# Performance work log

Measured on AMD Instinct MI355X. Metric: run time of the kernel, lower is better.

Reference implementation:

```python
import jax, jax.numpy as jnp
import numpy as np

WIN = 7          # window height/width
P = 10           # prompts_len
HEADS = 12
B0 = 32          # image batch (spa_prompts batch)
NW = 64          # windows per image
NW_TOK = WIN * WIN  # 49


def _relative_position_index(w):
    coords = np.stack(np.meshgrid(np.arange(w), np.arange(w), indexing='ij'))  # [2,w,w]
    flat = coords.reshape(2, -1)                        # [2, w*w]
    rel = flat[:, :, None] - flat[:, None, :]           # [2, w*w, w*w]
    rel = rel.transpose(1, 2, 0).astype(np.int64)       # [w*w, w*w, 2]
    rel[..., 0] += w - 1
    rel[..., 1] += w - 1
    rel[..., 0] *= 2 * w - 1
    return rel.sum(-1)                                  # [w*w, w*w]

REL_IDX = jnp.asarray(_relative_position_index(WIN))    # [49,49] int


def setup_inputs() -> dict:
    key = jax.random.key(0)
    ks = jax.random.split(key, 8)
    dim = 384
    return {
        'x': jax.random.normal(ks[0], (B0 * NW, NW_TOK, dim), jnp.float32),
        'spa_prompts': jax.random.normal(ks[1], (B0, P, dim), jnp.float32),
        'mask': jax.random.normal(ks[2], (NW, NW_TOK, NW_TOK), jnp.float32),
        'bias_table': jax.random.normal(ks[3], (169, HEADS), jnp.float32) * 0.02,
        'w_qkv': jax.random.normal(ks[4], (3 * dim, dim), jnp.float32) * 0.02,
        'b_qkv': jax.random.normal(ks[5], (3 * dim,), jnp.float32) * 0.02,
        'w_proj': jax.random.normal(ks[6], (dim, dim), jnp.float32) * 0.02,
        'b_proj': jax.random.normal(ks[7], (dim,), jnp.float32) * 0.02,
    }


def reference(x, spa_prompts, mask, bias_table, w_qkv, b_qkv, w_proj, b_proj):
    B_, Nw, C = x.shape
    b0 = spa_prompts.shape[0]
    nW = B_ // b0
    hd = C // HEADS
    scale = hd ** -0.5

    # broadcast prompts to every window and prepend
    prompts = jnp.broadcast_to(spa_prompts[:, None], (b0, nW, P, C)).reshape(B_, P, C)
    xc = jnp.concatenate([prompts, x], axis=1)          # [B_, N, C], N = P + Nw
    N = xc.shape[1]

    qkv = xc @ w_qkv.T + b_qkv                          # [B_, N, 3C]
    qkv = qkv.reshape(B_, N, 3, HEADS, hd).transpose(2, 0, 3, 1, 4)
    q, k, v = qkv[0], qkv[1], qkv[2]                    # [B_, H, N, hd]

    attn_weight = jnp.einsum('bhnd,bhmd->bhnm', q, k)   # unscaled, returned

    # relative position bias gathered for the window block, padded over prompt rows/cols
    rpb = bias_table[REL_IDX.reshape(-1)].reshape(NW_TOK, NW_TOK, HEADS)
    rpb = rpb.transpose(2, 0, 1)                        # [H, 49, 49]
    bias_full = jnp.pad(rpb, ((0, 0), (P, 0), (P, 0)))  # [H, N, N]

    attn = attn_weight * scale + bias_full[None]

    mask_full = jnp.pad(mask, ((0, 0), (P, 0), (P, 0)))  # [nW, N, N]
    attn = attn.reshape(b0, nW, HEADS, N, N) + mask_full[None, :, None]
    attn = jax.nn.softmax(attn.reshape(B_, HEADS, N, N), axis=-1)

    out = jnp.einsum('bhnm,bhmd->bnhd', attn, v).reshape(B_, N, C)
    out = out @ w_proj.T + b_proj

    prompts_out = out[:, :P].reshape(b0, nW, P, C).mean(axis=1)
    x_out = out[:, P:]
    return (x_out, attn_weight, prompts_out)
```

## Files before the change

kernel.cpp:

```cpp
#include <hip/hip_runtime.h>
#include <hip/hip_bf16.h>

#define P     10
#define NTOK  59
#define HEADS 12
#define NWTOK 49

#define AW_OFF 38535168
#define PO_OFF 124096512

typedef __attribute__((ext_vector_type(8))) short short8;
typedef __attribute__((ext_vector_type(8))) unsigned short ushort8;
typedef __attribute__((ext_vector_type(4))) float floatx4;
typedef unsigned int uint_g __attribute__((address_space(1)));
typedef unsigned int uint_l __attribute__((address_space(3)));

__device__ __forceinline__ unsigned short f2b(float f) {
  unsigned u = __builtin_bit_cast(unsigned, f);
  u += 0x7fffu + ((u >> 16) & 1u);
  return (unsigned short)(u >> 16);
}

__device__ __forceinline__ void gll16(const void* g, void* l) {
  __builtin_amdgcn_global_load_lds((const uint_g*)g, (uint_l*)l, 16, 0, 0);
}

__global__ __launch_bounds__(256) void convert_w_kernel(
    const float* __restrict__ w, unsigned short* __restrict__ wb) {
  const int i = (blockIdx.x * 256 + threadIdx.x) * 8;
  const float4 a = *(const float4*)(w + i);
  const float4 b = *(const float4*)(w + i + 4);
  ushort8 o;
  o[0] = f2b(a.x); o[1] = f2b(a.y); o[2] = f2b(a.z); o[3] = f2b(a.w);
  o[4] = f2b(b.x); o[5] = f2b(b.y); o[6] = f2b(b.z); o[7] = f2b(b.w);
  *(ushort8*)(wb + i) = o;
}

__global__ __launch_bounds__(256) void combo_kernel(
    const float* __restrict__ mask, const float* __restrict__ bias_table,
    float* __restrict__ combo) {
  const int bid = blockIdx.x;
  const int h = bid % HEADS, wnd = bid / HEADS;
  for (int e = threadIdx.x; e < 2401; e += 256) {
    const int ti = e / 49, tj = e - (e / 49) * 49;
    const int ai = ti / 7, aj = ti - ai * 7;
    const int bi = tj / 7, bj = tj - bi * 7;
    const int ridx = (ai - bi + 6) * 13 + (aj - bj + 6);
    combo[(size_t)bid * 2401 + e] =
        bias_table[ridx * HEADS + h] + mask[(size_t)wnd * 2401 + e];
  }
}

__global__ __launch_bounds__(256) void gather_x_kernel(
    const float* __restrict__ x, const float* __restrict__ spa,
    unsigned short* __restrict__ xc) {
  const int chunk = blockIdx.x * 256 + threadIdx.x;
  const int m = chunk / 48, kc = chunk - m * 48;
  const int b = m / 59, tok = m - b * 59;
  const float* src = (tok < P)
      ? spa + ((size_t)((b >> 6) * P + tok)) * 384 + kc * 8
      : x + ((size_t)(b * NWTOK + tok - P)) * 384 + kc * 8;
  const float4 v0 = ((const float4*)src)[0];
  const float4 v1 = ((const float4*)src)[1];
  ushort8 o;
  o[0] = f2b(v0.x); o[1] = f2b(v0.y); o[2] = f2b(v0.z); o[3] = f2b(v0.w);
  o[4] = f2b(v1.x); o[5] = f2b(v1.y); o[6] = f2b(v1.z); o[7] = f2b(v1.w);
  *(ushort8*)(xc + (size_t)m * 384 + kc * 8) = o;
}

__global__ __launch_bounds__(256) void gemm_qkv_kernel(
    const unsigned short* __restrict__ A, const unsigned short* __restrict__ Bw,
    const float* __restrict__ b_qkv, unsigned short* __restrict__ qkvw) {
  __shared__ unsigned short Asw[8192];
  __shared__ unsigned short Bsw[8192];
  const int t = threadIdx.x;
  const int w = t >> 6, lane = t & 63;
  const int lr = lane & 15, lg = lane >> 4;
  const int w0 = w >> 1, w1 = w & 1;
  const size_t m0 = (size_t)blockIdx.y * 128;
  const int n0 = blockIdx.x * 128;
  const int srow = lane >> 3, cpos = lane & 7;

  floatx4 acc[4][4];
#pragma unroll
  for (int mr = 0; mr < 4; ++mr)
#pragma unroll
    for (int nc = 0; nc < 4; ++nc) acc[mr][nc] = (floatx4)0.f;

  for (int k0 = 0; k0 < 384; k0 += 64) {
#pragma unroll
    for (int i = 0; i < 4; ++i) {
      const int r = (w * 4 + i) * 8 + srow;
      const int c = cpos ^ (r & 7);
      gll16(A + (m0 + r) * 384 + k0 + c * 8, Asw + (w * 4 + i) * 512);
      gll16(Bw + (size_t)(n0 + r) * 384 + k0 + c * 8, Bsw + (w * 4 + i) * 512);
    }
    __syncthreads();
#pragma unroll
    for (int kh = 0; kh < 2; ++kh) {
      short8 af[4], bf[4];
#pragma unroll
      for (int mr = 0; mr < 4; ++mr) {
        const int r = w0 * 64 + mr * 16 + lr;
        af[mr] = *(const short8*)(Asw + r * 64 + (((kh * 4 + lg) ^ (r & 7)) * 8));
      }
#pragma unroll
      for (int nc = 0; nc < 4; ++nc) {
        const int r = w1 * 64 + nc * 16 + lr;
        bf[nc] = *(const short8*)(Bsw + r * 64 + (((kh * 4 + lg) ^ (r & 7)) * 8));
      }
#pragma unroll
      for (int mr = 0; mr < 4; ++mr)
#pragma unroll
        for (int nc = 0; nc < 4; ++nc)
          acc[mr][nc] = __builtin_amdgcn_mfma_f32_16x16x32_bf16(
              af[mr], bf[nc], acc[mr][nc], 0, 0, 0);
    }
    __syncthreads();
  }

  const int sec = blockIdx.x / 3;
  float bias[4]; int hh[4], dd[4];
#pragma unroll
  for (int nc = 0; nc < 4; ++nc) {
    const int n = n0 + w1 * 64 + nc * 16 + lr;
    bias[nc] = b_qkv[n];
    hh[nc] = (n >> 5) % 12;
    dd[nc] = n & 31;
  }
#pragma unroll
  for (int mr = 0; mr < 4; ++mr)
#pragma unroll
    for (int reg = 0; reg < 4; ++reg) {
      const int m = (int)m0 + w0 * 64 + mr * 16 + lg * 4 + reg;
      const int bb = m / 59, tok = m - bb * 59;
      const size_t base = (size_t)(bb * 3 + sec) * 12 * 1888 + (size_t)tok * 32;
#pragma unroll
      for (int nc = 0; nc < 4; ++nc)
        qkvw[base + (size_t)hh[nc] * 1888 + dd[nc]] =
            f2b(acc[mr][nc][reg] + bias[nc]);
    }
}

__global__ __launch_bounds__(256) void attn_kernel(
    const unsigned short* __restrict__ qkvw, const float* __restrict__ combo,
    float* __restrict__ aw_out, unsigned short* __restrict__ attn_bf) {
  __shared__ char lds[31872];
  float* S = (float*)lds;
  unsigned short* qs = (unsigned short*)(lds + 16896);
  unsigned short* ks = (unsigned short*)(lds + 22016);
  unsigned short* vt = (unsigned short*)(lds + 27136);
  unsigned short* Pm = (unsigned short*)(lds + 16896);

  const int blk = blockIdx.x;
  const int b = blk / HEADS, h = blk - b * HEADS;
  const int t = threadIdx.x;
  const int w = t >> 6, lane = t & 63, lr = lane & 15, lg = lane >> 4;

  const size_t qoff = ((size_t)(b * 3 + 0) * 12 + h) * 1888;
  const size_t koff = ((size_t)(b * 3 + 1) * 12 + h) * 1888;
  const size_t voff = ((size_t)(b * 3 + 2) * 12 + h) * 1888;

  if (t < 236) {
    const int row = t >> 2, dc = (t & 3) * 8;
    const ushort8 q8 = *(const ushort8*)(qkvw + qoff + t * 8);
    const ushort8 k8 = *(const ushort8*)(qkvw + koff + t * 8);
    const ushort8 v8 = *(const ushort8*)(qkvw + voff + t * 8);
    *(ushort8*)(qs + row * 40 + dc) = q8;
    *(ushort8*)(ks + row * 40 + dc) = k8;
#pragma unroll
    for (int j = 0; j < 8; ++j) vt[(dc + j) * 74 + row] = v8[j];
  } else {
    const int e = t - 236;
#pragma unroll
    for (int jj = 0; jj < 8; ++jj) {
      const int f = e * 8 + jj;
      vt[(f / 5) * 74 + 59 + (f % 5)] = 0;
    }
  }
  __syncthreads();

  const short8 qa = *(const short8*)(qs + (w * 16 + lr) * 40 + lg * 8);
  const int q = w * 16 + lr;
  floatx4 sacc[4];
#pragma unroll
  for (int nt = 0; nt < 4; ++nt) {
    const short8 kb = *(const short8*)(ks + (nt * 16 + lr) * 40 + lg * 8);
    sacc[nt] = __builtin_amdgcn_mfma_f32_16x16x32_bf16(kb, qa, (floatx4)0.f, 0, 0, 0);
  }
#pragma unroll
  for (int nt = 0; nt < 4; ++nt)
#pragma unroll
    for (int reg = 0; reg < 4; ++reg)
      S[q * 66 + nt * 16 + lg * 4 + reg] = sacc[nt][reg];
  __syncthreads();

  float* aw = aw_out + (size_t)blk * (NTOK * NTOK);
  for (int idx = t; idx < NTOK * NTOK; idx += 256) {
    const int i = idx / 59, j = idx - i * 59;
    aw[idx] = S[i * 66 + j];
  }

  const float scale = 0.17677669529663687f;
  const float* comb = combo + (size_t)((b & 63) * HEADS + h) * 2401;
  float ev[4][4];
  float mx = -3.0e38f;
#pragma unroll
  for (int nt = 0; nt < 4; ++nt)
#pragma unroll
    for (int reg = 0; reg < 4; ++reg) {
      const int kk = nt * 16 + lg * 4 + reg;
      float v = -3.0e38f;
      if (q < NTOK && kk < NTOK) {
        const float cb = (q >= P && kk >= P) ? comb[(q - P) * 49 + (kk - P)] : 0.f;
        v = fmaf(sacc[nt][reg], scale, cb);
      }
      ev[nt][reg] = v;
      mx = fmaxf(mx, v);
    }
  mx = fmaxf(mx, __shfl_xor(mx, 16));
  mx = fmaxf(mx, __shfl_xor(mx, 32));
  float sm = 0.f;
#pragma unroll
  for (int nt = 0; nt < 4; ++nt)
#pragma unroll
    for (int reg = 0; reg < 4; ++reg) {
      const float e = __expf(ev[nt][reg] - mx);
      ev[nt][reg] = e;
      sm += e;
    }
  sm += __shfl_xor(sm, 16);
  sm += __shfl_xor(sm, 32);
  const float inv = 1.0f / sm;
#pragma unroll
  for (int nt = 0; nt < 4; ++nt) {
    uint2 uu;
    uu.x = (unsigned)f2b(ev[nt][0] * inv) | ((unsigned)f2b(ev[nt][1] * inv) << 16);
    uu.y = (unsigned)f2b(ev[nt][2] * inv) | ((unsigned)f2b(ev[nt][3] * inv) << 16);
    *(uint2*)(Pm + q * 72 + nt * 16 + lg * 4) = uu;
  }

  floatx4 oacc[2];
  oacc[0] = (floatx4)0.f; oacc[1] = (floatx4)0.f;
#pragma unroll
  for (int kk = 0; kk < 2; ++kk) {
    const short8 pa = *(const short8*)(Pm + (w * 16 + lr) * 72 + kk * 32 + lg * 8);
#pragma unroll
    for (int nt = 0; nt < 2; ++nt) {
      const short8 vb = *(const short8*)(vt + (nt * 16 + lr) * 74 + kk * 32 + lg * 8);
      oacc[nt] = __builtin_amdgcn_mfma_f32_16x16x32_bf16(pa, vb, oacc[nt], 0, 0, 0);
    }
  }
#pragma unroll
  for (int nt = 0; nt < 2; ++nt)
#pragma unroll
    for (int reg = 0; reg < 4; ++reg) {
      const int row = w * 16 + lg * 4 + reg;
      if (row < NTOK) {
        const int d = nt * 16 + lr;
        attn_bf[((size_t)(b * NTOK + row)) * 384 + h * 32 + d] = f2b(oacc[nt][reg]);
      }
    }
}

__global__ __launch_bounds__(256) void gemm_proj_kernel(
    const unsigned short* __restrict__ A, const unsigned short* __restrict__ Bw,
    const float* __restrict__ b_proj, float* __restrict__ x_out,
    float* __restrict__ pbuf) {
  __shared__ unsigned short Asw[8192];
  __shared__ unsigned short Bsw[8192];
  const int t = threadIdx.x;
  const int w = t >> 6, lane = t & 63;
  const int lr = lane & 15, lg = lane >> 4;
  const int w0 = w >> 1, w1 = w & 1;
  const size_t m0 = (size_t)blockIdx.y * 128;
  const int n0 = blockIdx.x * 128;
  const int srow = lane >> 3, cpos = lane & 7;

  floatx4 acc[4][4];
#pragma unroll
  for (int mr = 0; mr < 4; ++mr)
#pragma unroll
    for (int nc = 0; nc < 4; ++nc) acc[mr][nc] = (floatx4)0.f;

  for (int k0 = 0; k0 < 384; k0 += 64) {
#pragma unroll
    for (int i = 0; i < 4; ++i) {
      const int r = (w * 4 + i) * 8 + srow;
      const int c = cpos ^ (r & 7);
      gll16(A + (m0 + r) * 384 + k0 + c * 8, Asw + (w * 4 + i) * 512);
      gll16(Bw + (size_t)(n0 + r) * 384 + k0 + c * 8, Bsw + (w * 4 + i) * 512);
    }
    __syncthreads();
#pragma unroll
    for (int kh = 0; kh < 2; ++kh) {
      short8 af[4], bf[4];
#pragma unroll
      for (int mr = 0; mr < 4; ++mr) {
        const int r = w0 * 64 + mr * 16 + lr;
        af[mr] = *(const short8*)(Asw + r * 64 + (((kh * 4 + lg) ^ (r & 7)) * 8));
      }
#pragma unroll
      for (int nc = 0; nc < 4; ++nc) {
        const int r = w1 * 64 + nc * 16 + lr;
        bf[nc] = *(const short8*)(Bsw + r * 64 + (((kh * 4 + lg) ^ (r & 7)) * 8));
      }
#pragma unroll
      for (int mr = 0; mr < 4; ++mr)
#pragma unroll
        for (int nc = 0; nc < 4; ++nc)
          acc[mr][nc] = __builtin_amdgcn_mfma_f32_16x16x32_bf16(
              af[mr], bf[nc], acc[mr][nc], 0, 0, 0);
    }
    __syncthreads();
  }

  float bias[4]; int nn[4];
#pragma unroll
  for (int nc = 0; nc < 4; ++nc) {
    nn[nc] = n0 + w1 * 64 + nc * 16 + lr;
    bias[nc] = b_proj[nn[nc]];
  }
#pragma unroll
  for (int mr = 0; mr < 4; ++mr)
#pragma unroll
    for (int reg = 0; reg < 4; ++reg) {
      const int m = (int)m0 + w0 * 64 + mr * 16 + lg * 4 + reg;
      const int bb = m / 59, tok = m - bb * 59;
      float* dst = (tok >= P)
          ? x_out + (size_t)(bb * NWTOK + tok - P) * 384
          : pbuf + (size_t)(bb * P + tok) * 384;
#pragma unroll
      for (int nc = 0; nc < 4; ++nc)
        dst[nn[nc]] = acc[mr][nc][reg] + bias[nc];
    }
}

__global__ __launch_bounds__(256) void reduce_prompts_kernel(
    const float* __restrict__ pbuf, float* __restrict__ po) {
  const int o = blockIdx.x * 256 + threadIdx.x;
  const int b0 = o / 3840;
  const int rem = o - b0 * 3840;
  const float* base = pbuf + (size_t)b0 * 64 * 3840 + rem;
  float s = 0.f;
#pragma unroll 8
  for (int w = 0; w < 64; ++w) s += base[(size_t)w * 3840];
  po[o] = s * (1.f / 64.f);
}

extern "C" void kernel_launch(void* const* d_in, const int* in_sizes, int n_in,
                              void* d_out, int out_size, void* d_ws, size_t ws_size,
                              hipStream_t stream) {
  const float* x          = (const float*)d_in[0];
  const float* spa        = (const float*)d_in[1];
  const float* mask       = (const float*)d_in[2];
  const float* bias_table = (const float*)d_in[3];
  const float* w_qkv      = (const float*)d_in[4];
  const float* b_qkv      = (const float*)d_in[5];
  const float* w_proj     = (const float*)d_in[6];
  const float* b_proj     = (const float*)d_in[7];
  float* out = (float*)d_out;

  unsigned short* xc_bf    = (unsigned short*)d_ws;
  unsigned short* attn_bf  = xc_bf;
  unsigned short* qkvw     = (unsigned short*)((char*)d_ws + 92798976ULL);
  unsigned short* wqkv_bf  = (unsigned short*)((char*)d_ws + 371195904ULL);
  unsigned short* wproj_bf = (unsigned short*)((char*)d_ws + 372080640ULL);
  float*          pbuf     = (float*)((char*)d_ws + 372375552ULL);
  float*          combo    = (float*)((char*)d_ws + 403832832ULL);

  convert_w_kernel<<<216, 256, 0, stream>>>(w_qkv, wqkv_bf);
  convert_w_kernel<<<72, 256, 0, stream>>>(w_proj, wproj_bf);
  combo_kernel<<<768, 256, 0, stream>>>(mask, bias_table, combo);
  gather_x_kernel<<<22656, 256, 0, stream>>>(x, spa, xc_bf);
  gemm_qkv_kernel<<<dim3(9, 944), 256, 0, stream>>>(xc_bf, wqkv_bf, b_qkv, qkvw);
  attn_kernel<<<2048 * HEADS, 256, 0, stream>>>(qkvw, combo, out + AW_OFF, attn_bf);
  gemm_proj_kernel<<<dim3(3, 944), 256, 0, stream>>>(attn_bf, wproj_bf, b_proj,
                                                     out, pbuf);
  reduce_prompts_kernel<<<480, 256, 0, stream>>>(pbuf, out + PO_OFF);
}
```

Baseline: 604.4 us.

## Compute prompt QKV once per image instead of per window, write outputs directly

The QKV GEMM no longer runs on prompt tokens replicated across all 64 windows. It computes x tokens and the 320 unique prompt rows separately into two layouts, and the attention kernel reads prompt q/k/v from the shared per-image buffer. The attention kernel also writes the fp32 attn_weight rows straight from MFMA registers, dropping the LDS staging and its extra barrier, and stages the bf16 output through LDS so global stores are 16-byte. The cost is more branching and address logic in both kernels, plus a partially wasted tile for the prompt rows.

```diff
diff --git a/kernel.cpp b/kernel.cpp
--- a/kernel.cpp
+++ b/kernel.cpp
@@ -12,6 +12,7 @@
 typedef __attribute__((ext_vector_type(8))) short short8;
 typedef __attribute__((ext_vector_type(8))) unsigned short ushort8;
 typedef __attribute__((ext_vector_type(4))) float floatx4;
+typedef float f4u __attribute__((ext_vector_type(4), aligned(4)));
 typedef unsigned int uint_g __attribute__((address_space(1)));
 typedef unsigned int uint_l __attribute__((address_space(3)));
 
@@ -51,33 +52,18 @@
   }
 }
 
-__global__ __launch_bounds__(256) void gather_x_kernel(
-    const float* __restrict__ x, const float* __restrict__ spa,
-    unsigned short* __restrict__ xc) {
-  const int chunk = blockIdx.x * 256 + threadIdx.x;
-  const int m = chunk / 48, kc = chunk - m * 48;
-  const int b = m / 59, tok = m - b * 59;
-  const float* src = (tok < P)
-      ? spa + ((size_t)((b >> 6) * P + tok)) * 384 + kc * 8
-      : x + ((size_t)(b * NWTOK + tok - P)) * 384 + kc * 8;
-  const float4 v0 = ((const float4*)src)[0];
-  const float4 v1 = ((const float4*)src)[1];
-  ushort8 o;
-  o[0] = f2b(v0.x); o[1] = f2b(v0.y); o[2] = f2b(v0.z); o[3] = f2b(v0.w);
-  o[4] = f2b(v1.x); o[5] = f2b(v1.y); o[6] = f2b(v1.z); o[7] = f2b(v1.w);
-  *(ushort8*)(xc + (size_t)m * 384 + kc * 8) = o;
-}
-
 __global__ __launch_bounds__(256) void gemm_qkv_kernel(
-    const unsigned short* __restrict__ A, const unsigned short* __restrict__ Bw,
-    const float* __restrict__ b_qkv, unsigned short* __restrict__ qkvw) {
+    const unsigned short* __restrict__ xb, const unsigned short* __restrict__ xp,
+    const unsigned short* __restrict__ Bw, const float* __restrict__ b_qkv,
+    unsigned short* __restrict__ qkx, unsigned short* __restrict__ qkp) {
   __shared__ unsigned short Asw[8192];
   __shared__ unsigned short Bsw[8192];
   const int t = threadIdx.x;
   const int w = t >> 6, lane = t & 63;
   const int lr = lane & 15, lg = lane >> 4;
   const int w0 = w >> 1, w1 = w & 1;
-  const size_t m0 = (size_t)blockIdx.y * 128;
+  const int by = blockIdx.y;
+  const bool isP = by >= 784;
   const int n0 = blockIdx.x * 128;
   const int srow = lane >> 3, cpos = lane & 7;
 
@@ -92,7 +78,15 @@
     for (int i = 0; i < 4; ++i) {
       const int r = (w * 4 + i) * 8 + srow;
       const int c = cpos ^ (r & 7);
-      gll16(A + (m0 + r) * 384 + k0 + c * 8, Asw + (w * 4 + i) * 512);
+      const unsigned short* asrc;
+      if (!isP) {
+        asrc = xb + (size_t)(by * 128 + r) * 384 + k0 + c * 8;
+      } else {
+        int mp = (by - 784) * 128 + r;
+        if (mp > 319) mp = 319;
+        asrc = xp + (size_t)mp * 384 + k0 + c * 8;
+      }
+      gll16(asrc, Asw + (w * 4 + i) * 512);
       gll16(Bw + (size_t)(n0 + r) * 384 + k0 + c * 8, Bsw + (w * 4 + i) * 512);
     }
     __syncthreads();
@@ -132,40 +126,60 @@
   for (int mr = 0; mr < 4; ++mr)
 #pragma unroll
     for (int reg = 0; reg < 4; ++reg) {
-      const int m = (int)m0 + w0 * 64 + mr * 16 + lg * 4 + reg;
-      const int bb = m / 59, tok = m - bb * 59;
-      const size_t base = (size_t)(bb * 3 + sec) * 12 * 1888 + (size_t)tok * 32;
-#pragma unroll
-      for (int nc = 0; nc < 4; ++nc)
-        qkvw[base + (size_t)hh[nc] * 1888 + dd[nc]] =
-            f2b(acc[mr][nc][reg] + bias[nc]);
+      const int rloc = w0 * 64 + mr * 16 + lg * 4 + reg;
+      if (!isP) {
+        const int m = by * 128 + rloc;
+        const int bb = m / 49, tok = m - bb * 49;
+        const size_t base = (size_t)(bb * 3 + sec) * 12 * 1568 + (size_t)tok * 32;
+#pragma unroll
+        for (int nc = 0; nc < 4; ++nc)
+          qkx[base + (size_t)hh[nc] * 1568 + dd[nc]] =
+              f2b(acc[mr][nc][reg] + bias[nc]);
+      } else {
+        const int mp = (by - 784) * 128 + rloc;
+        if (mp < 320) {
+          const int b0 = mp / 10, ptok = mp - b0 * 10;
+          const size_t base = (size_t)(b0 * 3 + sec) * 12 * 320 + (size_t)ptok * 32;
+#pragma unroll
+          for (int nc = 0; nc < 4; ++nc)
+            qkp[base + (size_t)hh[nc] * 320 + dd[nc]] =
+                f2b(acc[mr][nc][reg] + bias[nc]);
+        }
+      }
     }
 }
 
 __global__ __launch_bounds__(256) void attn_kernel(
-    const unsigned short* __restrict__ qkvw, const float* __restrict__ combo,
-    float* __restrict__ aw_out, unsigned short* __restrict__ attn_bf) {
-  __shared__ char lds[31872];
-  float* S = (float*)lds;
-  unsigned short* qs = (unsigned short*)(lds + 16896);
-  unsigned short* ks = (unsigned short*)(lds + 22016);
-  unsigned short* vt = (unsigned short*)(lds + 27136);
-  unsigned short* Pm = (unsigned short*)(lds + 16896);
+    const unsigned short* __restrict__ qkx, const unsigned short* __restrict__ qkp,
+    const float* __restrict__ combo, float* __restrict__ aw_out,
+    unsigned short* __restrict__ attn_bf) {
+  __shared__ char lds[14976];
+  unsigned short* qs = (unsigned short*)(lds);
+  unsigned short* ks = (unsigned short*)(lds + 5120);
+  unsigned short* vt = (unsigned short*)(lds + 10240);
+  unsigned short* Pm = (unsigned short*)(lds);
 
   const int blk = blockIdx.x;
   const int b = blk / HEADS, h = blk - b * HEADS;
   const int t = threadIdx.x;
   const int w = t >> 6, lane = t & 63, lr = lane & 15, lg = lane >> 4;
 
-  const size_t qoff = ((size_t)(b * 3 + 0) * 12 + h) * 1888;
-  const size_t koff = ((size_t)(b * 3 + 1) * 12 + h) * 1888;
-  const size_t voff = ((size_t)(b * 3 + 2) * 12 + h) * 1888;
-
   if (t < 236) {
     const int row = t >> 2, dc = (t & 3) * 8;
-    const ushort8 q8 = *(const ushort8*)(qkvw + qoff + t * 8);
-    const ushort8 k8 = *(const ushort8*)(qkvw + koff + t * 8);
-    const ushort8 v8 = *(const ushort8*)(qkvw + voff + t * 8);
+    ushort8 q8, k8, v8;
+    if (row < P) {
+      const size_t base =
+          ((size_t)((b >> 6) * 3) * 12 + h) * 320 + row * 32 + dc;
+      q8 = *(const ushort8*)(qkp + base);
+      k8 = *(const ushort8*)(qkp + base + 12 * 320);
+      v8 = *(const ushort8*)(qkp + base + 24 * 320);
+    } else {
+      const size_t base =
+          ((size_t)(b * 3) * 12 + h) * 1568 + (row - P) * 32 + dc;
+      q8 = *(const ushort8*)(qkx + base);
+      k8 = *(const ushort8*)(qkx + base + 12 * 1568);
+      v8 = *(const ushort8*)(qkx + base + 24 * 1568);
+    }
     *(ushort8*)(qs + row * 40 + dc) = q8;
     *(ushort8*)(ks + row * 40 + dc) = k8;
 #pragma unroll
@@ -180,25 +194,27 @@
   }
   __syncthreads();
 
-  const short8 qa = *(const short8*)(qs + (w * 16 + lr) * 40 + lg * 8);
   const int q = w * 16 + lr;
+  const short8 qa = *(const short8*)(qs + q * 40 + lg * 8);
   floatx4 sacc[4];
 #pragma unroll
   for (int nt = 0; nt < 4; ++nt) {
     const short8 kb = *(const short8*)(ks + (nt * 16 + lr) * 40 + lg * 8);
     sacc[nt] = __builtin_amdgcn_mfma_f32_16x16x32_bf16(kb, qa, (floatx4)0.f, 0, 0, 0);
   }
-#pragma unroll
-  for (int nt = 0; nt < 4; ++nt)
-#pragma unroll
-    for (int reg = 0; reg < 4; ++reg)
-      S[q * 66 + nt * 16 + lg * 4 + reg] = sacc[nt][reg];
-  __syncthreads();
-
-  float* aw = aw_out + (size_t)blk * (NTOK * NTOK);
-  for (int idx = t; idx < NTOK * NTOK; idx += 256) {
-    const int i = idx / 59, j = idx - i * 59;
-    aw[idx] = S[i * 66 + j];
+
+  if (q < NTOK) {
+    float* rowp = aw_out + (size_t)blk * 3481 + q * 59;
+#pragma unroll
+    for (int nt = 0; nt < 3; ++nt)
+      *(f4u*)(rowp + nt * 16 + lg * 4) = __builtin_bit_cast(f4u, sacc[nt]);
+    if (lg < 2) {
+      *(f4u*)(rowp + 48 + lg * 4) = __builtin_bit_cast(f4u, sacc[3]);
+    } else if (lg == 2) {
+      rowp[56] = sacc[3][0];
+      rowp[57] = sacc[3][1];
+      rowp[58] = sacc[3][2];
+    }
   }
 
   const float scale = 0.17677669529663687f;
@@ -232,6 +248,8 @@
   sm += __shfl_xor(sm, 16);
   sm += __shfl_xor(sm, 32);
   const float inv = 1.0f / sm;
+
+  __syncthreads();
 #pragma unroll
   for (int nt = 0; nt < 4; ++nt) {
     uint2 uu;
@@ -251,16 +269,19 @@
       oacc[nt] = __builtin_amdgcn_mfma_f32_16x16x32_bf16(pa, vb, oacc[nt], 0, 0, 0);
     }
   }
+
+  unsigned short* wb = Pm + w * 1152;
 #pragma unroll
   for (int nt = 0; nt < 2; ++nt)
 #pragma unroll
-    for (int reg = 0; reg < 4; ++reg) {
-      const int row = w * 16 + lg * 4 + reg;
-      if (row < NTOK) {
-        const int d = nt * 16 + lr;
-        attn_bf[((size_t)(b * NTOK + row)) * 384 + h * 32 + d] = f2b(oacc[nt][reg]);
-      }
-    }
+    for (int reg = 0; reg < 4; ++reg)
+      wb[(lg * 4 + reg) * 40 + nt * 16 + lr] = f2b(oacc[nt][reg]);
+  const int rr = lane >> 2, c8 = (lane & 3) * 8;
+  const int row = w * 16 + rr;
+  if (row < NTOK) {
+    const ushort8 ov = *(const ushort8*)(wb + rr * 40 + c8);
+    *(ushort8*)(attn_bf + ((size_t)(b * NTOK + row)) * 384 + h * 32 + c8) = ov;
+  }
 }
 
 __global__ __launch_bounds__(256) void gemm_proj_kernel(
@@ -361,20 +382,25 @@
   const float* b_proj     = (const float*)d_in[7];
   float* out = (float*)d_out;
 
-  unsigned short* xc_bf    = (unsigned short*)d_ws;
-  unsigned short* attn_bf  = xc_bf;
-  unsigned short* qkvw     = (unsigned short*)((char*)d_ws + 92798976ULL);
-  unsigned short* wqkv_bf  = (unsigned short*)((char*)d_ws + 371195904ULL);
-  unsigned short* wproj_bf = (unsigned short*)((char*)d_ws + 372080640ULL);
-  float*          pbuf     = (float*)((char*)d_ws + 372375552ULL);
-  float*          combo    = (float*)((char*)d_ws + 403832832ULL);
-
+  unsigned short* x_bf     = (unsigned short*)d_ws;
+  unsigned short* attn_bf  = (unsigned short*)d_ws;
+  unsigned short* xp_bf    = (unsigned short*)((char*)d_ws + 77070336ULL);
+  unsigned short* wqkv_bf  = (unsigned short*)((char*)d_ws + 77316096ULL);
+  unsigned short* qkx      = (unsigned short*)((char*)d_ws + 92798976ULL);
+  unsigned short* qkp      = (unsigned short*)((char*)d_ws + 324009984ULL);
+  unsigned short* wproj_bf = (unsigned short*)((char*)d_ws + 324747264ULL);
+  float*          pbuf     = (float*)((char*)d_ws + 325042176ULL);
+  float*          combo    = (float*)((char*)d_ws + 356499456ULL);
+
+  convert_w_kernel<<<18816, 256, 0, stream>>>(x, x_bf);
+  convert_w_kernel<<<60, 256, 0, stream>>>(spa, xp_bf);
   convert_w_kernel<<<216, 256, 0, stream>>>(w_qkv, wqkv_bf);
   convert_w_kernel<<<72, 256, 0, stream>>>(w_proj, wproj_bf);
   combo_kernel<<<768, 256, 0, stream>>>(mask, bias_table, combo);
-  gather_x_kernel<<<22656, 256, 0, stream>>>(x, spa, xc_bf);
-  gemm_qkv_kernel<<<dim3(9, 944), 256, 0, stream>>>(xc_bf, wqkv_bf, b_qkv, qkvw);
-  attn_kernel<<<2048 * HEADS, 256, 0, stream>>>(qkvw, combo, out + AW_OFF, attn_bf);
+  gemm_qkv_kernel<<<dim3(9, 787), 256, 0, stream>>>(x_bf, xp_bf, wqkv_bf, b_qkv,
+                                                    qkx, qkp);
+  attn_kernel<<<2048 * HEADS, 256, 0, stream>>>(qkx, qkp, combo, out + AW_OFF,
+                                                attn_bf);
   gemm_proj_kernel<<<dim3(3, 944), 256, 0, stream>>>(attn_bf, wproj_bf, b_proj,
                                                      out, pbuf);
   reduce_prompts_kernel<<<480, 256, 0, stream>>>(pbuf, out + PO_OFF);
```

After: 594.1 us. Within noise of the previous version (-1.7%).

## Fuse input gather, QKV GEMM and attention into one per-window kernel

Applied to the files above, without the earlier changes.

Replaces the separate gather, QKV GEMM and per-head attention kernels with one kernel per window (512 threads). It converts the window's tokens to bf16 in LDS, streams the QKV weights through double-buffered LDS, and keeps Q/K/V in LDS for two rounds of six heads. This removes the large bf16 xc and qkv intermediates written to and read back from global memory, plus two launches. The trade is heavy LDS use (about 85 KB) and many accumulator registers, which may limit occupancy. Each block also rereads the full weight matrix, so weight reuse across windows now comes only from cache.

```diff
diff --git a/kernel.cpp b/kernel.cpp
--- a/kernel.cpp
+++ b/kernel.cpp
@@ -12,6 +12,7 @@
 typedef __attribute__((ext_vector_type(8))) short short8;
 typedef __attribute__((ext_vector_type(8))) unsigned short ushort8;
 typedef __attribute__((ext_vector_type(4))) float floatx4;
+typedef float f4u __attribute__((ext_vector_type(4), aligned(4)));
 typedef unsigned int uint_g __attribute__((address_space(1)));
 typedef unsigned int uint_l __attribute__((address_space(3)));
 
@@ -51,216 +52,243 @@
   }
 }
 
-__global__ __launch_bounds__(256) void gather_x_kernel(
+__global__ __launch_bounds__(512, 2) void fused_qkv_attn_kernel(
     const float* __restrict__ x, const float* __restrict__ spa,
-    unsigned short* __restrict__ xc) {
-  const int chunk = blockIdx.x * 256 + threadIdx.x;
-  const int m = chunk / 48, kc = chunk - m * 48;
-  const int b = m / 59, tok = m - b * 59;
-  const float* src = (tok < P)
-      ? spa + ((size_t)((b >> 6) * P + tok)) * 384 + kc * 8
-      : x + ((size_t)(b * NWTOK + tok - P)) * 384 + kc * 8;
-  const float4 v0 = ((const float4*)src)[0];
-  const float4 v1 = ((const float4*)src)[1];
-  ushort8 o;
-  o[0] = f2b(v0.x); o[1] = f2b(v0.y); o[2] = f2b(v0.z); o[3] = f2b(v0.w);
-  o[4] = f2b(v1.x); o[5] = f2b(v1.y); o[6] = f2b(v1.z); o[7] = f2b(v1.w);
-  *(ushort8*)(xc + (size_t)m * 384 + kc * 8) = o;
-}
-
-__global__ __launch_bounds__(256) void gemm_qkv_kernel(
-    const unsigned short* __restrict__ A, const unsigned short* __restrict__ Bw,
-    const float* __restrict__ b_qkv, unsigned short* __restrict__ qkvw) {
-  __shared__ unsigned short Asw[8192];
-  __shared__ unsigned short Bsw[8192];
-  const int t = threadIdx.x;
-  const int w = t >> 6, lane = t & 63;
-  const int lr = lane & 15, lg = lane >> 4;
-  const int w0 = w >> 1, w1 = w & 1;
-  const size_t m0 = (size_t)blockIdx.y * 128;
-  const int n0 = blockIdx.x * 128;
-  const int srow = lane >> 3, cpos = lane & 7;
-
-  floatx4 acc[4][4];
-#pragma unroll
-  for (int mr = 0; mr < 4; ++mr)
-#pragma unroll
-    for (int nc = 0; nc < 4; ++nc) acc[mr][nc] = (floatx4)0.f;
-
-  for (int k0 = 0; k0 < 384; k0 += 64) {
-#pragma unroll
-    for (int i = 0; i < 4; ++i) {
-      const int r = (w * 4 + i) * 8 + srow;
-      const int c = cpos ^ (r & 7);
-      gll16(A + (m0 + r) * 384 + k0 + c * 8, Asw + (w * 4 + i) * 512);
-      gll16(Bw + (size_t)(n0 + r) * 384 + k0 + c * 8, Bsw + (w * 4 + i) * 512);
-    }
-    __syncthreads();
-#pragma unroll
-    for (int kh = 0; kh < 2; ++kh) {
-      short8 af[4], bf[4];
-#pragma unroll
-      for (int mr = 0; mr < 4; ++mr) {
-        const int r = w0 * 64 + mr * 16 + lr;
-        af[mr] = *(const short8*)(Asw + r * 64 + (((kh * 4 + lg) ^ (r & 7)) * 8));
-      }
-#pragma unroll
-      for (int nc = 0; nc < 4; ++nc) {
-        const int r = w1 * 64 + nc * 16 + lr;
-        bf[nc] = *(const short8*)(Bsw + r * 64 + (((kh * 4 + lg) ^ (r & 7)) * 8));
-      }
-#pragma unroll
-      for (int mr = 0; mr < 4; ++mr)
-#pragma unroll
-        for (int nc = 0; nc < 4; ++nc)
-          acc[mr][nc] = __builtin_amdgcn_mfma_f32_16x16x32_bf16(
-              af[mr], bf[nc], acc[mr][nc], 0, 0, 0);
-    }
-    __syncthreads();
-  }
-
-  const int sec = blockIdx.x / 3;
-  float bias[4]; int hh[4], dd[4];
-#pragma unroll
-  for (int nc = 0; nc < 4; ++nc) {
-    const int n = n0 + w1 * 64 + nc * 16 + lr;
-    bias[nc] = b_qkv[n];
-    hh[nc] = (n >> 5) % 12;
-    dd[nc] = n & 31;
-  }
-#pragma unroll
-  for (int mr = 0; mr < 4; ++mr)
-#pragma unroll
-    for (int reg = 0; reg < 4; ++reg) {
-      const int m = (int)m0 + w0 * 64 + mr * 16 + lg * 4 + reg;
-      const int bb = m / 59, tok = m - bb * 59;
-      const size_t base = (size_t)(bb * 3 + sec) * 12 * 1888 + (size_t)tok * 32;
-#pragma unroll
-      for (int nc = 0; nc < 4; ++nc)
-        qkvw[base + (size_t)hh[nc] * 1888 + dd[nc]] =
-            f2b(acc[mr][nc][reg] + bias[nc]);
-    }
-}
-
-__global__ __launch_bounds__(256) void attn_kernel(
-    const unsigned short* __restrict__ qkvw, const float* __restrict__ combo,
-    float* __restrict__ aw_out, unsigned short* __restrict__ attn_bf) {
-  __shared__ char lds[31872];
-  float* S = (float*)lds;
-  unsigned short* qs = (unsigned short*)(lds + 16896);
-  unsigned short* ks = (unsigned short*)(lds + 22016);
-  unsigned short* vt = (unsigned short*)(lds + 27136);
-  unsigned short* Pm = (unsigned short*)(lds + 16896);
-
-  const int blk = blockIdx.x;
-  const int b = blk / HEADS, h = blk - b * HEADS;
+    const unsigned short* __restrict__ wqb, const float* __restrict__ b_qkv,
+    const float* __restrict__ combo, float* __restrict__ aw_out,
+    unsigned short* __restrict__ attn_bf) {
+  __shared__ char lds[87040];
+  unsigned short* xs   = (unsigned short*)lds;
+  unsigned short* wstA = (unsigned short*)(lds + 50176);
+  unsigned short* wstB = (unsigned short*)(lds + 66560);
+  unsigned short* q_l  = (unsigned short*)lds;
+  unsigned short* k_l  = (unsigned short*)(lds + 25600);
+  unsigned short* vt   = (unsigned short*)(lds + 51200);
+  unsigned short* obuf = (unsigned short*)(lds + 78848);
+
+  const int b = blockIdx.x;
   const int t = threadIdx.x;
   const int w = t >> 6, lane = t & 63, lr = lane & 15, lg = lane >> 4;
-
-  const size_t qoff = ((size_t)(b * 3 + 0) * 12 + h) * 1888;
-  const size_t koff = ((size_t)(b * 3 + 1) * 12 + h) * 1888;
-  const size_t voff = ((size_t)(b * 3 + 2) * 12 + h) * 1888;
-
-  if (t < 236) {
-    const int row = t >> 2, dc = (t & 3) * 8;
-    const ushort8 q8 = *(const ushort8*)(qkvw + qoff + t * 8);
-    const ushort8 k8 = *(const ushort8*)(qkvw + koff + t * 8);
-    const ushort8 v8 = *(const ushort8*)(qkvw + voff + t * 8);
-    *(ushort8*)(qs + row * 40 + dc) = q8;
-    *(ushort8*)(ks + row * 40 + dc) = k8;
-#pragma unroll
-    for (int j = 0; j < 8; ++j) vt[(dc + j) * 74 + row] = v8[j];
-  } else {
-    const int e = t - 236;
-#pragma unroll
-    for (int jj = 0; jj < 8; ++jj) {
-      const int f = e * 8 + jj;
-      vt[(f / 5) * 74 + 59 + (f % 5)] = 0;
-    }
+  const int rB = w * 16 + lr;
+
+#pragma unroll
+  for (int ci = 0; ci < 6; ++ci) {
+    const int e = ci * 4096 + t * 8;
+    const int r = e / 384, c = e - r * 384;
+    ushort8 o;
+    if (r < NTOK) {
+      const float* src = (r < P)
+          ? spa + ((size_t)((b >> 6) * P + r)) * 384 + c
+          : x + ((size_t)(b * NWTOK + r - P)) * 384 + c;
+      const float4 v0 = ((const float4*)src)[0];
+      const float4 v1 = ((const float4*)src)[1];
+      o[0] = f2b(v0.x); o[1] = f2b(v0.y); o[2] = f2b(v0.z); o[3] = f2b(v0.w);
+      o[4] = f2b(v1.x); o[5] = f2b(v1.y); o[6] = f2b(v1.z); o[7] = f2b(v1.w);
+    } else {
+      o = (ushort8)0;
+    }
+    *(ushort8*)(xs + r * 392 + c) = o;
+  }
+
+#pragma unroll
+  for (int i = 0; i < 2; ++i) {
+    const int g = w * 2 + i;
+    const int r = g * 8 + (lane >> 3);
+    const int c = (lane & 7) ^ (r & 7);
+    gll16(wqb + (size_t)r * 384 + c * 8, wstA + g * 512);
   }
   __syncthreads();
 
-  const short8 qa = *(const short8*)(qs + (w * 16 + lr) * 40 + lg * 8);
-  const int q = w * 16 + lr;
-  floatx4 sacc[4];
-#pragma unroll
-  for (int nt = 0; nt < 4; ++nt) {
-    const short8 kb = *(const short8*)(ks + (nt * 16 + lr) * 40 + lg * 8);
-    sacc[nt] = __builtin_amdgcn_mfma_f32_16x16x32_bf16(kb, qa, (floatx4)0.f, 0, 0, 0);
-  }
-#pragma unroll
-  for (int nt = 0; nt < 4; ++nt)
-#pragma unroll
-    for (int reg = 0; reg < 4; ++reg)
-      S[q * 66 + nt * 16 + lg * 4 + reg] = sacc[nt][reg];
-  __syncthreads();
-
-  float* aw = aw_out + (size_t)blk * (NTOK * NTOK);
-  for (int idx = t; idx < NTOK * NTOK; idx += 256) {
-    const int i = idx / 59, j = idx - i * 59;
-    aw[idx] = S[i * 66 + j];
-  }
-
+  floatx4 acc[9][4];
+#pragma unroll
+  for (int n9 = 0; n9 < 9; ++n9)
+#pragma unroll
+    for (int mt = 0; mt < 4; ++mt) acc[n9][mt] = (floatx4)0.f;
+
+  short8 af[2][4];
+#pragma unroll
+  for (int s = 0; s < 54; ++s) {
+    const int kz = s / 9, nt9 = s % 9;
+    unsigned short* cur = (s & 1) ? wstB : wstA;
+    unsigned short* nxt = (s & 1) ? wstA : wstB;
+    if (nt9 == 0) {
+#pragma unroll
+      for (int kk = 0; kk < 2; ++kk)
+#pragma unroll
+        for (int mt = 0; mt < 4; ++mt)
+          af[kk][mt] = *(const short8*)(xs + (mt * 16 + lr) * 392 + kz * 64 +
+                                        kk * 32 + lg * 8);
+    }
+    if (s < 53) {
+      const int s1 = s + 1, kz1 = s1 / 9, nt1 = s1 % 9;
+#pragma unroll
+      for (int i = 0; i < 2; ++i) {
+        const int g = w * 2 + i;
+        const int r = g * 8 + (lane >> 3);
+        const int c = (lane & 7) ^ (r & 7);
+        gll16(wqb + (size_t)(nt1 * 128 + r) * 384 + kz1 * 64 + c * 8,
+              nxt + g * 512);
+      }
+    }
+#pragma unroll
+    for (int kk = 0; kk < 2; ++kk) {
+      const short8 bf =
+          *(const short8*)(cur + rB * 64 + (((kk * 4 + lg) ^ (rB & 7)) * 8));
+#pragma unroll
+      for (int mt = 0; mt < 4; ++mt)
+        acc[nt9][mt] = __builtin_amdgcn_mfma_f32_16x16x32_bf16(
+            af[kk][mt], bf, acc[nt9][mt], 0, 0, 0);
+    }
+    __syncthreads();
+  }
+
+  float bias9[9];
+#pragma unroll
+  for (int i = 0; i < 9; ++i) bias9[i] = b_qkv[i * 128 + w * 16 + lr];
+  const int d_sc = (w & 1) * 16 + lr;
+  const int hw = w >> 1;
   const float scale = 0.17677669529663687f;
-  const float* comb = combo + (size_t)((b & 63) * HEADS + h) * 2401;
-  float ev[4][4];
-  float mx = -3.0e38f;
-#pragma unroll
-  for (int nt = 0; nt < 4; ++nt)
-#pragma unroll
-    for (int reg = 0; reg < 4; ++reg) {
-      const int kk = nt * 16 + lg * 4 + reg;
-      float v = -3.0e38f;
-      if (q < NTOK && kk < NTOK) {
-        const float cb = (q >= P && kk >= P) ? comb[(q - P) * 49 + (kk - P)] : 0.f;
-        v = fmaf(sacc[nt][reg], scale, cb);
-      }
-      ev[nt][reg] = v;
-      mx = fmaxf(mx, v);
-    }
-  mx = fmaxf(mx, __shfl_xor(mx, 16));
-  mx = fmaxf(mx, __shfl_xor(mx, 32));
-  float sm = 0.f;
-#pragma unroll
-  for (int nt = 0; nt < 4; ++nt)
-#pragma unroll
-    for (int reg = 0; reg < 4; ++reg) {
-      const float e = __expf(ev[nt][reg] - mx);
-      ev[nt][reg] = e;
-      sm += e;
-    }
-  sm += __shfl_xor(sm, 16);
-  sm += __shfl_xor(sm, 32);
-  const float inv = 1.0f / sm;
-#pragma unroll
-  for (int nt = 0; nt < 4; ++nt) {
-    uint2 uu;
-    uu.x = (unsigned)f2b(ev[nt][0] * inv) | ((unsigned)f2b(ev[nt][1] * inv) << 16);
-    uu.y = (unsigned)f2b(ev[nt][2] * inv) | ((unsigned)f2b(ev[nt][3] * inv) << 16);
-    *(uint2*)(Pm + q * 72 + nt * 16 + lg * 4) = uu;
-  }
-
-  floatx4 oacc[2];
-  oacc[0] = (floatx4)0.f; oacc[1] = (floatx4)0.f;
-#pragma unroll
-  for (int kk = 0; kk < 2; ++kk) {
-    const short8 pa = *(const short8*)(Pm + (w * 16 + lr) * 72 + kk * 32 + lg * 8);
-#pragma unroll
-    for (int nt = 0; nt < 2; ++nt) {
-      const short8 vb = *(const short8*)(vt + (nt * 16 + lr) * 74 + kk * 32 + lg * 8);
-      oacc[nt] = __builtin_amdgcn_mfma_f32_16x16x32_bf16(pa, vb, oacc[nt], 0, 0, 0);
-    }
-  }
-#pragma unroll
-  for (int nt = 0; nt < 2; ++nt)
-#pragma unroll
-    for (int reg = 0; reg < 4; ++reg) {
-      const int row = w * 16 + lg * 4 + reg;
-      if (row < NTOK) {
-        const int d = nt * 16 + lr;
-        attn_bf[((size_t)(b * NTOK + row)) * 384 + h * 32 + d] = f2b(oacc[nt][reg]);
-      }
-    }
+
+#pragma unroll
+  for (int rnd = 0; rnd < 2; ++rnd) {
+#pragma unroll
+    for (int nt9 = 0; nt9 < 9; ++nt9) {
+      const int sec = nt9 / 3;
+      const int h = (nt9 % 3) * 4 + hw;
+      if ((h >= 6 ? 1 : 0) == rnd) {
+        const int hl = h - rnd * 6;
+#pragma unroll
+        for (int mt = 0; mt < 4; ++mt) {
+          if (sec == 2) {
+#pragma unroll
+            for (int pp = 0; pp < 2; ++pp) {
+              const int m = mt * 16 + lg * 4 + pp * 2;
+              const unsigned u =
+                  (unsigned)f2b(acc[nt9][mt][pp * 2] + bias9[nt9]) |
+                  ((unsigned)f2b(acc[nt9][mt][pp * 2 + 1] + bias9[nt9]) << 16);
+              *(unsigned*)(vt + hl * 2304 + d_sc * 72 + m) = u;
+            }
+          } else {
+            unsigned short* dst = (sec == 0) ? q_l : k_l;
+#pragma unroll
+            for (int reg = 0; reg < 4; ++reg) {
+              const int m = mt * 16 + lg * 4 + reg;
+              dst[m * 200 + hl * 32 + d_sc] = f2b(acc[nt9][mt][reg] + bias9[nt9]);
+            }
+          }
+        }
+      }
+    }
+    __syncthreads();
+
+#pragma unroll
+    for (int i = 0; i < 3; ++i) {
+      const int tau = w * 3 + i;
+      const int hl = tau >> 2, qw = tau & 3;
+      const int hg = rnd * 6 + hl;
+      const int q = qw * 16 + lr;
+
+      const short8 qa = *(const short8*)(q_l + q * 200 + hl * 32 + lg * 8);
+      floatx4 sacc[4];
+#pragma unroll
+      for (int nt = 0; nt < 4; ++nt) {
+        const short8 kb =
+            *(const short8*)(k_l + (nt * 16 + lr) * 200 + hl * 32 + lg * 8);
+        sacc[nt] = __builtin_amdgcn_mfma_f32_16x16x32_bf16(kb, qa, (floatx4)0.f,
+                                                           0, 0, 0);
+      }
+      if (q < NTOK) {
+        float* rowp = aw_out + ((size_t)(b * HEADS + hg)) * 3481 + q * 59;
+#pragma unroll
+        for (int nt = 0; nt < 3; ++nt)
+          *(f4u*)(rowp + nt * 16 + lg * 4) = __builtin_bit_cast(f4u, sacc[nt]);
+        if (lg < 2) {
+          *(f4u*)(rowp + 48 + lg * 4) = __builtin_bit_cast(f4u, sacc[3]);
+        } else if (lg == 2) {
+          rowp[56] = sacc[3][0]; rowp[57] = sacc[3][1]; rowp[58] = sacc[3][2];
+        }
+      }
+
+      const float* comb = combo + (size_t)((b & 63) * HEADS + hg) * 2401;
+      float ev[4][4];
+      float mx = -3.0e38f;
+#pragma unroll
+      for (int nt = 0; nt < 4; ++nt)
+#pragma unroll
+        for (int reg = 0; reg < 4; ++reg) {
+          const int kk2 = nt * 16 + lg * 4 + reg;
+          float v = -3.0e38f;
+          if (q < NTOK && kk2 < NTOK) {
+            const float cb =
+                (q >= P && kk2 >= P) ? comb[(q - P) * 49 + (kk2 - P)] : 0.f;
+            v = fmaf(sacc[nt][reg], scale, cb);
+          }
+          ev[nt][reg] = v;
+          mx = fmaxf(mx, v);
+        }
+      mx = fmaxf(mx, __shfl_xor(mx, 16));
+      mx = fmaxf(mx, __shfl_xor(mx, 32));
+      float sm = 0.f;
+#pragma unroll
+      for (int nt = 0; nt < 4; ++nt)
+#pragma unroll
+        for (int reg = 0; reg < 4; ++reg) {
+          const float e = __expf(ev[nt][reg] - mx);
+          ev[nt][reg] = e;
+          sm += e;
+        }
+      sm += __shfl_xor(sm, 16);
+      sm += __shfl_xor(sm, 32);
+      const float inv = 1.0f / sm;
+
+      unsigned pk[4][2];
+#pragma unroll
+      for (int nt = 0; nt < 4; ++nt)
+#pragma unroll
+        for (int pp = 0; pp < 2; ++pp)
+          pk[nt][pp] = (unsigned)f2b(ev[nt][2 * pp] * inv) |
+                       ((unsigned)f2b(ev[nt][2 * pp + 1] * inv) << 16);
+
+      floatx4 oacc[2];
+      oacc[0] = (floatx4)0.f; oacc[1] = (floatx4)0.f;
+#pragma unroll
+      for (int kk = 0; kk < 2; ++kk) {
+        unsigned W4[4];
+#pragma unroll
+        for (int jp = 0; jp < 4; ++jp) {
+          const int srcl = lr + 16 * (2 * (lg & 1) + (jp >> 1));
+          const int lo = __shfl((int)pk[2 * kk][jp & 1], srcl);
+          const int hi = __shfl((int)pk[2 * kk + 1][jp & 1], srcl);
+          W4[jp] = (lg >> 1) ? (unsigned)hi : (unsigned)lo;
+        }
+        uint4 wu; wu.x = W4[0]; wu.y = W4[1]; wu.z = W4[2]; wu.w = W4[3];
+        const short8 pa = __builtin_bit_cast(short8, wu);
+#pragma unroll
+        for (int nt = 0; nt < 2; ++nt) {
+          const short8 vb = *(const short8*)(vt + hl * 2304 +
+                                             (nt * 16 + lr) * 72 + kk * 32 +
+                                             lg * 8);
+          oacc[nt] =
+              __builtin_amdgcn_mfma_f32_16x16x32_bf16(pa, vb, oacc[nt], 0, 0, 0);
+        }
+      }
+
+      unsigned short* wb = obuf + w * 512;
+#pragma unroll
+      for (int nt = 0; nt < 2; ++nt)
+#pragma unroll
+        for (int reg = 0; reg < 4; ++reg)
+          wb[(lg * 4 + reg) * 32 + nt * 16 + lr] = f2b(oacc[nt][reg]);
+      const int rr = lane >> 2, cc = (lane & 3) * 8;
+      const int qg = qw * 16 + rr;
+      if (qg < NTOK) {
+        const ushort8 ov = *(const ushort8*)(wb + rr * 32 + cc);
+        *(ushort8*)(attn_bf + ((size_t)(b * NTOK + qg)) * 384 + hg * 32 + cc) =
+            ov;
+      }
+    }
+    __syncthreads();
+  }
 }
 
 __global__ __launch_bounds__(256) void gemm_proj_kernel(
@@ -361,20 +389,17 @@
   const float* b_proj     = (const float*)d_in[7];
   float* out = (float*)d_out;
 
-  unsigned short* xc_bf    = (unsigned short*)d_ws;
-  unsigned short* attn_bf  = xc_bf;
-  unsigned short* qkvw     = (unsigned short*)((char*)d_ws + 92798976ULL);
-  unsigned short* wqkv_bf  = (unsigned short*)((char*)d_ws + 371195904ULL);
-  unsigned short* wproj_bf = (unsigned short*)((char*)d_ws + 372080640ULL);
-  float*          pbuf     = (float*)((char*)d_ws + 372375552ULL);
-  float*          combo    = (float*)((char*)d_ws + 403832832ULL);
+  unsigned short* attn_bf  = (unsigned short*)d_ws;
+  unsigned short* wqkv_bf  = (unsigned short*)((char*)d_ws + 92798976ULL);
+  unsigned short* wproj_bf = (unsigned short*)((char*)d_ws + 93683712ULL);
+  float*          pbuf     = (float*)((char*)d_ws + 93978624ULL);
+  float*          combo    = (float*)((char*)d_ws + 125435904ULL);
 
   convert_w_kernel<<<216, 256, 0, stream>>>(w_qkv, wqkv_bf);
   convert_w_kernel<<<72, 256, 0, stream>>>(w_proj, wproj_bf);
   combo_kernel<<<768, 256, 0, stream>>>(mask, bias_table, combo);
-  gather_x_kernel<<<22656, 256, 0, stream>>>(x, spa, xc_bf);
-  gemm_qkv_kernel<<<dim3(9, 944), 256, 0, stream>>>(xc_bf, wqkv_bf, b_qkv, qkvw);
-  attn_kernel<<<2048 * HEADS, 256, 0, stream>>>(qkvw, combo, out + AW_OFF, attn_bf);
+  fused_qkv_attn_kernel<<<2048, 512, 0, stream>>>(
+      x, spa, wqkv_bf, b_qkv, combo, out + AW_OFF, attn_bf);
   gemm_proj_kernel<<<dim3(3, 944), 256, 0, stream>>>(attn_bf, wproj_bf, b_proj,
                                                      out, pbuf);
   reduce_prompts_kernel<<<480, 256, 0, stream>>>(pbuf, out + PO_OFF);
```

Measured after the change: 633.1 us. 1.05x slower.
